# Optimization experiments

Measured on AMD Instinct MI355X. Metric: run time of the kernel, lower is better.

The kernel has to match this reference:

```python
import jax, jax.numpy as jnp
import numpy as np

C = 64          # num_channels
DEPTH = 9       # dilation_depth
REPEAT = 2      # dilation_repeat
K = 2           # kernel_size
DILATIONS = [2 ** j for _ in range(REPEAT) for j in range(DEPTH)]
L = len(DILATIONS)  # 18 gated layers


def causal_conv(x, w, b, dilation):
    # x: [B, Cin, T], w: [Cout, Cin, K] -> [B, Cout, T] with causal (left) padding
    pad = (w.shape[-1] - 1) * dilation
    y = jax.lax.conv_general_dilated(
        x, w, window_strides=(1,), padding=[(pad, 0)],
        rhs_dilation=(dilation,), dimension_numbers=("NCH", "OIH", "NCH"))
    return y + b[None, :, None]


def setup_inputs() -> dict:
    key = jax.random.key(0)
    ks = jax.random.split(key, 9)
    s = 0.1
    x = jax.random.normal(ks[0], (4, 1, 65536), dtype=jnp.float32)
    in_w = jax.random.normal(ks[1], (C, 1, 1), dtype=jnp.float32) * s
    in_b = jax.random.normal(ks[2], (C,), dtype=jnp.float32) * s
    hid_w = jax.random.normal(ks[3], (L, 2 * C, C, K), dtype=jnp.float32) * s
    hid_b = jax.random.normal(ks[4], (L, 2 * C), dtype=jnp.float32) * s
    res_w = jax.random.normal(ks[5], (L, C, C, 1), dtype=jnp.float32) * s
    res_b = jax.random.normal(ks[6], (L, C), dtype=jnp.float32) * s
    mix_w = jax.random.normal(ks[7], (1, C * L, 1), dtype=jnp.float32) * s
    mix_b = jax.random.normal(ks[8], (1,), dtype=jnp.float32) * s
    return {"x": x, "in_w": in_w, "in_b": in_b, "hid_w": hid_w, "hid_b": hid_b,
            "res_w": res_w, "res_b": res_b, "mix_w": mix_w, "mix_b": mix_b}


def reference(x, in_w, in_b, hid_w, hid_b, res_w, res_b, mix_w, mix_b):
    # Input 1x1 conv: [B,1,T] -> [B,C,T]
    out = causal_conv(x, in_w, in_b, 1)
    skips = []
    for i, d in enumerate(DILATIONS):
        xi = out
        h = causal_conv(xi, hid_w[i], hid_b[i], d)       # [B, 2C, T]
        gated = jnp.tanh(h[:, :C]) * jax.nn.sigmoid(h[:, C:])  # [B, C, T]
        skips.append(gated)
        out = causal_conv(gated, res_w[i], res_b[i], 1) + xi    # residual
    skip = jnp.concatenate(skips, axis=1)                # [B, C*L, T]
    return causal_conv(skip, mix_w, mix_b, 1)            # [B, 1, T]
```

## Files before the change

### kernel.cpp

```cpp
#include <hip/hip_runtime.h>
#include <hip/hip_bf16.h>
#include <math.h>

#define NCH 64
#define T_LEN 65536
#define NLAYER 18

typedef __attribute__((ext_vector_type(8))) short bf16x8;
typedef __attribute__((ext_vector_type(4))) short bf16x4;
typedef __attribute__((ext_vector_type(4))) float f32x4;

static __device__ __forceinline__ float bf2f(short s) {
    union { short u[2]; float f; } v;
    v.u[0] = 0; v.u[1] = s;
    return v.f;
}
static __device__ __forceinline__ short f2bf(float f) {
    __hip_bfloat16 h = __float2bfloat16(f);
    return *(short*)&h;
}

__global__ void convert_weights_kernel(const float* __restrict__ hid_w,
                                       const float* __restrict__ res_w,
                                       __hip_bfloat16* __restrict__ whid,
                                       __hip_bfloat16* __restrict__ wres) {
    int gid = blockIdx.x * 256 + threadIdx.x;
    if (gid < NLAYER * 128 * 128) {
        int l   = gid >> 14;
        int rem = gid & 16383;
        int o   = rem >> 7;
        int k   = rem & 127;
        float v = (k < 64)
            ? hid_w[((l * 128 + o) * 64 + k) * 2]
            : hid_w[((l * 128 + o) * 64 + (k - 64)) * 2 + 1];
        whid[gid] = __float2bfloat16(v);
    }
    if (gid < NLAYER * 64 * 64) {
        wres[gid] = __float2bfloat16(res_w[gid]);
    }
}

__global__ __launch_bounds__(256, 2) void fused6_kernel(
    const void* __restrict__ src,
    __hip_bfloat16* __restrict__ next,
    float* __restrict__ acc,
    const __hip_bfloat16* __restrict__ whid_all,
    const float* __restrict__ hb_all,
    const __hip_bfloat16* __restrict__ wres_all,
    const float* __restrict__ rb_all,
    const float* __restrict__ mix_w,
    const float* __restrict__ in_w,
    const float* __restrict__ in_b,
    int lbase, int is_first) {
    __shared__ __align__(16) __hip_bfloat16 A[192 * 72];
    __shared__ __align__(16) __hip_bfloat16 G[192 * 72];

    const int b    = blockIdx.x >> 9;
    const int widx = blockIdx.x & 511;
    const int t0   = widx << 7;
    const int tw   = t0 - 64;

    const int tid  = threadIdx.x;
    const int lane = tid & 63;
    const int w4   = tid >> 6;
    const int l15  = lane & 15;
    const int quad = lane >> 4;
    const int m0   = w4 * 16;
    const int rr   = tid >> 3;
    const int co   = (tid & 7) * 8;

    if (is_first) {
        const float* x = (const float*)src;
        float iw[8], ib[8];
#pragma unroll
        for (int j = 0; j < 8; ++j) { iw[j] = in_w[co + j]; ib[j] = in_b[co + j]; }
#pragma unroll
        for (int round = 0; round < 6; ++round) {
            int r  = round * 32 + rr;
            int gt = tw + r;
            bf16x8 v = {0, 0, 0, 0, 0, 0, 0, 0};
            if (gt >= 0) {
                float xv = x[(size_t)b * T_LEN + gt];
#pragma unroll
                for (int j = 0; j < 8; ++j) v[j] = f2bf(iw[j] * xv + ib[j]);
            }
            *(bf16x8*)(&A[r * 72 + co]) = v;
        }
    } else {
        const __hip_bfloat16* prev = (const __hip_bfloat16*)src;
#pragma unroll
        for (int round = 0; round < 6; ++round) {
            int r  = round * 32 + rr;
            int gt = tw + r;
            bf16x8 v = {0, 0, 0, 0, 0, 0, 0, 0};
            if (gt >= 0)
                v = *(const bf16x8*)(prev + ((size_t)b * T_LEN + gt) * NCH + co);
            *(bf16x8*)(&A[r * 72 + co]) = v;
        }
    }

    float skacc0 = 0.f, skacc1 = 0.f;

#pragma unroll 1
    for (int l = 0; l < 6; ++l) {
        const int d = 1 << l;
        const __hip_bfloat16* whid = whid_all + (size_t)(lbase + l) * 16384;
        const __hip_bfloat16* wres = wres_all + (size_t)(lbase + l) * 4096;
        const float* hb = hb_all + (lbase + l) * 128;
        const float* rb = rb_all + (lbase + l) * 64;
        const float* mw = mix_w + (lbase + l) * 64;

        bf16x8 aT[4], aS[4], aR[2];
        {
            const __hip_bfloat16* whT = whid + (size_t)(m0 + l15) * 128 + quad * 8;
            const __hip_bfloat16* whS = whT + 64 * 128;
#pragma unroll
            for (int k = 0; k < 4; ++k) {
                aT[k] = *(const bf16x8*)(whT + k * 32);
                aS[k] = *(const bf16x8*)(whS + k * 32);
            }
            const __hip_bfloat16* wrA = wres + (size_t)(m0 + l15) * 64 + quad * 8;
            aR[0] = *(const bf16x8*)(wrA);
            aR[1] = *(const bf16x8*)(wrA + 32);
        }
        f32x4 biasT, biasS, biasR;
#pragma unroll
        for (int r = 0; r < 4; ++r) {
            biasT[r] = hb[m0 + quad * 4 + r];
            biasS[r] = hb[64 + m0 + quad * 4 + r];
            biasR[r] = rb[m0 + quad * 4 + r];
        }
        float mwq[16];
#pragma unroll
        for (int k = 0; k < 4; ++k) {
            float4 m4 = *(const float4*)(mw + quad * 16 + k * 4);
            mwq[k * 4 + 0] = m4.x; mwq[k * 4 + 1] = m4.y;
            mwq[k * 4 + 2] = m4.z; mwq[k * 4 + 3] = m4.w;
        }

        __syncthreads();

#pragma unroll
        for (int ct = 0; ct < 3; ++ct) {
            f32x4 accT[4], accS[4];
#pragma unroll
            for (int nt = 0; nt < 4; ++nt) { accT[nt] = biasT; accS[nt] = biasS; }
#pragma unroll
            for (int ks = 0; ks < 4; ++ks) {
                const int koff = (ks & 1) * 32 + quad * 8;
#pragma unroll
                for (int nt = 0; nt < 4; ++nt) {
                    int trow = ct * 64 + nt * 16 + l15;
                    int prow = trow - d;  prow = prow < 0 ? 0 : prow;
                    int row  = (ks < 2) ? prow : trow;
                    bf16x8 bx = *(const bf16x8*)(&A[row * 72 + koff]);
                    accT[nt] = __builtin_amdgcn_mfma_f32_16x16x32_bf16(aT[ks], bx, accT[nt], 0, 0, 0);
                    accS[nt] = __builtin_amdgcn_mfma_f32_16x16x32_bf16(aS[ks], bx, accS[nt], 0, 0, 0);
                }
            }
#pragma unroll
            for (int nt = 0; nt < 4; ++nt) {
                int trow = ct * 64 + nt * 16 + l15;
                bf16x4 gv;
#pragma unroll
                for (int r = 0; r < 4; ++r) {
                    float e2 = __expf(2.f * accT[nt][r]);
                    float th = 1.f - 2.f * __builtin_amdgcn_rcpf(e2 + 1.f);
                    float sg = __builtin_amdgcn_rcpf(1.f + __expf(-accS[nt][r]));
                    gv[r] = f2bf(th * sg);
                }
                *(bf16x4*)(&G[trow * 72 + m0 + quad * 4]) = gv;
            }
        }
        __syncthreads();

#pragma unroll
        for (int ct = 0; ct < 3; ++ct) {
            f32x4 accR[4];
#pragma unroll
            for (int nt = 0; nt < 4; ++nt) accR[nt] = biasR;
#pragma unroll
            for (int ks = 0; ks < 2; ++ks) {
                const int koff = ks * 32 + quad * 8;
#pragma unroll
                for (int nt = 0; nt < 4; ++nt) {
                    int trow = ct * 64 + nt * 16 + l15;
                    bf16x8 bx = *(const bf16x8*)(&G[trow * 72 + koff]);
                    accR[nt] = __builtin_amdgcn_mfma_f32_16x16x32_bf16(aR[ks], bx, accR[nt], 0, 0, 0);
                }
            }
#pragma unroll
            for (int nt = 0; nt < 4; ++nt) {
                int trow = ct * 64 + nt * 16 + l15;
                bf16x4 old = *(const bf16x4*)(&A[trow * 72 + m0 + quad * 4]);
                bool ok = (tw + trow) >= 0;
                bf16x4 ov;
#pragma unroll
                for (int r = 0; r < 4; ++r) {
                    float v = accR[nt][r] + bf2f(old[r]);
                    ov[r] = f2bf(ok ? v : 0.f);
                }
                *(bf16x4*)(&A[trow * 72 + m0 + quad * 4]) = ov;
            }
        }

#pragma unroll
        for (int s = 0; s < 2; ++s) {
            int p = 64 + w4 * 32 + s * 16 + l15;
            bf16x8 g0 = *(const bf16x8*)(&G[p * 72 + quad * 16]);
            bf16x8 g1 = *(const bf16x8*)(&G[p * 72 + quad * 16 + 8]);
            float sv = 0.f;
#pragma unroll
            for (int j = 0; j < 8; ++j) {
                sv += mwq[j]     * bf2f(g0[j]);
                sv += mwq[8 + j] * bf2f(g1[j]);
            }
            if (s == 0) skacc0 += sv; else skacc1 += sv;
        }
    }
    __syncthreads();

#pragma unroll
    for (int round = 0; round < 4; ++round) {
        int pr = round * 32 + rr;
        *(bf16x8*)(next + ((size_t)b * T_LEN + t0 + pr) * NCH + co) =
            *(const bf16x8*)(&A[(pr + 64) * 72 + co]);
    }

    skacc0 += __shfl_xor(skacc0, 16, 64);
    skacc0 += __shfl_xor(skacc0, 32, 64);
    skacc1 += __shfl_xor(skacc1, 16, 64);
    skacc1 += __shfl_xor(skacc1, 32, 64);
    if (quad == 0) {
        acc[(size_t)b * T_LEN + t0 + w4 * 32 + l15]      += skacc0;
        acc[(size_t)b * T_LEN + t0 + w4 * 32 + 16 + l15] += skacc1;
    }
}

__global__ __launch_bounds__(256, 2) void layer_mfma_kernel(
    const __hip_bfloat16* __restrict__ prev,
    __hip_bfloat16* __restrict__ next,
    float* __restrict__ acc,
    const __hip_bfloat16* __restrict__ whid,
    const float* __restrict__ hb,
    const __hip_bfloat16* __restrict__ wres,
    const float* __restrict__ rb,
    const float* __restrict__ mw,
    int d) {
    __shared__ __align__(16) __hip_bfloat16 Xp[64 * 72];
    __shared__ __align__(16) __hip_bfloat16 Xc[64 * 72];
    __shared__ __align__(16) __hip_bfloat16 Gt[64 * 72];

    const int t0   = blockIdx.x << 6;
    const int tid  = threadIdx.x;
    const int lane = tid & 63;
    const int w4   = tid >> 6;
    const int l15  = lane & 15;
    const int quad = lane >> 4;
    const int m0   = w4 * 16;
    const int rr = tid >> 3;
    const int co = (tid & 7) * 8;

    bf16x8 aT[4], aS[4], aR[2];
    {
        const __hip_bfloat16* whT = whid + (size_t)(m0 + l15) * 128 + quad * 8;
        const __hip_bfloat16* whS = whT + 64 * 128;
#pragma unroll
        for (int k = 0; k < 4; ++k) {
            aT[k] = *(const bf16x8*)(whT + k * 32);
            aS[k] = *(const bf16x8*)(whS + k * 32);
        }
        const __hip_bfloat16* wrA = wres + (size_t)(m0 + l15) * 64 + quad * 8;
        aR[0] = *(const bf16x8*)(wrA);
        aR[1] = *(const bf16x8*)(wrA + 32);
    }
    f32x4 biasT, biasS, biasR;
#pragma unroll
    for (int r = 0; r < 4; ++r) {
        biasT[r] = hb[m0 + quad * 4 + r];
        biasS[r] = hb[64 + m0 + quad * 4 + r];
        biasR[r] = rb[m0 + quad * 4 + r];
    }
    float mwq[16];
#pragma unroll
    for (int j = 0; j < 16; ++j) mwq[j] = mw[quad * 16 + j];

    bf16x8 pc[2], pp[2];
#define LOAD_TILE(b)                                                          \
    do {                                                                      \
        const __hip_bfloat16* pb = prev + ((size_t)(b) * T_LEN + t0) * NCH;   \
        _Pragma("unroll")                                                     \
        for (int pass = 0; pass < 2; ++pass) {                                \
            int r = pass * 32 + rr;                                           \
            pc[pass] = *(const bf16x8*)(pb + r * NCH + co);                   \
            int tp = t0 + r - d;                                              \
            bf16x8 z = {0, 0, 0, 0, 0, 0, 0, 0};                              \
            pp[pass] = z;                                                     \
            if (tp >= 0)                                                      \
                pp[pass] = *(const bf16x8*)(prev +                            \
                    ((size_t)(b) * T_LEN + tp) * NCH + co);                   \
        }                                                                     \
    } while (0)

    LOAD_TILE(0);

#pragma unroll
    for (int b = 0; b < 4; ++b) {
#pragma unroll
        for (int pass = 0; pass < 2; ++pass) {
            int r = pass * 32 + rr;
            *(bf16x8*)(&Xc[r * 72 + co]) = pc[pass];
            *(bf16x8*)(&Xp[r * 72 + co]) = pp[pass];
        }
        __syncthreads();

        if (b < 3) LOAD_TILE(b + 1);

        f32x4 accT[4], accS[4];
#pragma unroll
        for (int nt = 0; nt < 4; ++nt) { accT[nt] = biasT; accS[nt] = biasS; }
#pragma unroll
        for (int ks = 0; ks < 4; ++ks) {
            const __hip_bfloat16* srcb = (ks < 2) ? Xp : Xc;
            const int kk = (ks & 1) * 32 + quad * 8;
#pragma unroll
            for (int nt = 0; nt < 4; ++nt) {
                bf16x8 bx = *(const bf16x8*)(&srcb[(nt * 16 + l15) * 72 + kk]);
                accT[nt] = __builtin_amdgcn_mfma_f32_16x16x32_bf16(aT[ks], bx, accT[nt], 0, 0, 0);
                accS[nt] = __builtin_amdgcn_mfma_f32_16x16x32_bf16(aS[ks], bx, accS[nt], 0, 0, 0);
            }
        }

#pragma unroll
        for (int nt = 0; nt < 4; ++nt) {
            int t = nt * 16 + l15;
#pragma unroll
            for (int r = 0; r < 4; ++r) {
                float e2 = __expf(2.f * accT[nt][r]);
                float th = 1.f - 2.f * __builtin_amdgcn_rcpf(e2 + 1.f);
                float sg = __builtin_amdgcn_rcpf(1.f + __expf(-accS[nt][r]));
                Gt[t * 72 + m0 + quad * 4 + r] = __float2bfloat16(th * sg);
            }
        }

        bf16x4 curres[4];
#pragma unroll
        for (int nt = 0; nt < 4; ++nt) {
            curres[nt] = *(const bf16x4*)(&Xc[(nt * 16 + l15) * 72 + m0 + quad * 4]);
        }
        __syncthreads();

        f32x4 accR[4];
#pragma unroll
        for (int nt = 0; nt < 4; ++nt) accR[nt] = biasR;
#pragma unroll
        for (int ks = 0; ks < 2; ++ks) {
            const int kk = ks * 32 + quad * 8;
#pragma unroll
            for (int nt = 0; nt < 4; ++nt) {
                bf16x8 bx = *(const bf16x8*)(&Gt[(nt * 16 + l15) * 72 + kk]);
                accR[nt] = __builtin_amdgcn_mfma_f32_16x16x32_bf16(aR[ks], bx, accR[nt], 0, 0, 0);
            }
        }

        __hip_bfloat16* nb = next + ((size_t)b * T_LEN + t0) * NCH;
#pragma unroll
        for (int nt = 0; nt < 4; ++nt) {
            int t = nt * 16 + l15;
            bf16x4 ov;
#pragma unroll
            for (int r = 0; r < 4; ++r) {
                ov[r] = f2bf(accR[nt][r] + bf2f(curres[nt][r]));
            }
            *(bf16x4*)(nb + t * NCH + m0 + quad * 4) = ov;
        }

        {
            int t = w4 * 16 + l15;
            bf16x8 g0 = *(const bf16x8*)(&Gt[t * 72 + quad * 16]);
            bf16x8 g1 = *(const bf16x8*)(&Gt[t * 72 + quad * 16 + 8]);
            float s = 0.f;
#pragma unroll
            for (int j = 0; j < 8; ++j) {
                s += mwq[j]     * bf2f(g0[j]);
                s += mwq[8 + j] * bf2f(g1[j]);
            }
            s += __shfl_xor(s, 16, 64);
            s += __shfl_xor(s, 32, 64);
            if (quad == 0)
                acc[(size_t)b * T_LEN + t0 + t] += s;
        }
    }
#undef LOAD_TILE
}

__global__ __launch_bounds__(256, 2) void last_layer_kernel(
    const __hip_bfloat16* __restrict__ prev,
    const float* __restrict__ acc,
    float* __restrict__ out,
    const __hip_bfloat16* __restrict__ whid,
    const float* __restrict__ hb,
    const float* __restrict__ mw,
    const float* __restrict__ mix_b,
    int d) {
    __shared__ __align__(16) __hip_bfloat16 Xp[64 * 72];
    __shared__ __align__(16) __hip_bfloat16 Xc[64 * 72];
    __shared__ float skb[4 * 64];

    const int t0   = blockIdx.x << 6;
    const int tid  = threadIdx.x;
    const int lane = tid & 63;
    const int w4   = tid >> 6;
    const int l15  = lane & 15;
    const int quad = lane >> 4;
    const int m0   = w4 * 16;
    const int rr = tid >> 3;
    const int co = (tid & 7) * 8;

    bf16x8 aT[4], aS[4];
    {
        const __hip_bfloat16* whT = whid + (size_t)(m0 + l15) * 128 + quad * 8;
        const __hip_bfloat16* whS = whT + 64 * 128;
#pragma unroll
        for (int k = 0; k < 4; ++k) {
            aT[k] = *(const bf16x8*)(whT + k * 32);
            aS[k] = *(const bf16x8*)(whS + k * 32);
        }
    }
    f32x4 biasT, biasS;
    float mwv[4];
#pragma unroll
    for (int r = 0; r < 4; ++r) {
        biasT[r] = hb[m0 + quad * 4 + r];
        biasS[r] = hb[64 + m0 + quad * 4 + r];
        mwv[r]   = mw[m0 + quad * 4 + r];
    }
    const float mb = mix_b[0];

    bf16x8 pc[2], pp[2];
#define LOAD_TILE(b)                                                          \
    do {                                                                      \
        const __hip_bfloat16* pb = prev + ((size_t)(b) * T_LEN + t0) * NCH;   \
        _Pragma("unroll")                                                     \
        for (int pass = 0; pass < 2; ++pass) {                                \
            int r = pass * 32 + rr;                                           \
            pc[pass] = *(const bf16x8*)(pb + r * NCH + co);                   \
            int tp = t0 + r - d;                                              \
            bf16x8 z = {0, 0, 0, 0, 0, 0, 0, 0};                              \
            pp[pass] = z;                                                     \
            if (tp >= 0)                                                      \
                pp[pass] = *(const bf16x8*)(prev +                            \
                    ((size_t)(b) * T_LEN + tp) * NCH + co);                   \
        }                                                                     \
    } while (0)

    LOAD_TILE(0);

#pragma unroll
    for (int b = 0; b < 4; ++b) {
#pragma unroll
        for (int pass = 0; pass < 2; ++pass) {
            int r = pass * 32 + rr;
            *(bf16x8*)(&Xc[r * 72 + co]) = pc[pass];
            *(bf16x8*)(&Xp[r * 72 + co]) = pp[pass];
        }
        __syncthreads();

        if (b < 3) LOAD_TILE(b + 1);

        f32x4 accT[4], accS[4];
#pragma unroll
        for (int nt = 0; nt < 4; ++nt) { accT[nt] = biasT; accS[nt] = biasS; }
#pragma unroll
        for (int ks = 0; ks < 4; ++ks) {
            const __hip_bfloat16* srcb = (ks < 2) ? Xp : Xc;
            const int kk = (ks & 1) * 32 + quad * 8;
#pragma unroll
            for (int nt = 0; nt < 4; ++nt) {
                bf16x8 bx = *(const bf16x8*)(&srcb[(nt * 16 + l15) * 72 + kk]);
                accT[nt] = __builtin_amdgcn_mfma_f32_16x16x32_bf16(aT[ks], bx, accT[nt], 0, 0, 0);
                accS[nt] = __builtin_amdgcn_mfma_f32_16x16x32_bf16(aS[ks], bx, accS[nt], 0, 0, 0);
            }
        }

#pragma unroll
        for (int nt = 0; nt < 4; ++nt) {
            float sv = 0.f;
#pragma unroll
            for (int r = 0; r < 4; ++r) {
                float e2 = __expf(2.f * accT[nt][r]);
                float th = 1.f - 2.f * __builtin_amdgcn_rcpf(e2 + 1.f);
                float sg = __builtin_amdgcn_rcpf(1.f + __expf(-accS[nt][r]));
                sv += mwv[r] * (th * sg);
            }
            sv += __shfl_xor(sv, 16, 64);
            sv += __shfl_xor(sv, 32, 64);
            if (quad == 0)
                skb[w4 * 64 + nt * 16 + l15] = sv;
        }
        __syncthreads();

        if (tid < 64) {
            float tot = skb[tid] + skb[64 + tid] + skb[128 + tid] + skb[192 + tid];
            out[(size_t)b * T_LEN + t0 + tid] =
                acc[(size_t)b * T_LEN + t0 + tid] + tot + mb;
        }
    }
#undef LOAD_TILE
}

extern "C" void kernel_launch(void* const* d_in, const int* in_sizes, int n_in,
                              void* d_out, int out_size, void* d_ws, size_t ws_size,
                              hipStream_t stream) {
    const float* x     = (const float*)d_in[0];
    const float* in_w  = (const float*)d_in[1];
    const float* in_b  = (const float*)d_in[2];
    const float* hid_w = (const float*)d_in[3];
    const float* hid_b = (const float*)d_in[4];
    const float* res_w = (const float*)d_in[5];
    const float* res_b = (const float*)d_in[6];
    const float* mix_w = (const float*)d_in[7];
    const float* mix_b = (const float*)d_in[8];
    float* out = (float*)d_out;

    const size_t act_elems = 4ull * T_LEN * NCH;
    __hip_bfloat16* actA = (__hip_bfloat16*)d_ws;
    __hip_bfloat16* actB = actA + act_elems;
    float* acc = (float*)(actB + act_elems);
    __hip_bfloat16* whid = (__hip_bfloat16*)(acc + 4ull * T_LEN);
    __hip_bfloat16* wres = whid + (size_t)NLAYER * 128 * 128;

    hipMemsetAsync(acc, 0, 4ull * T_LEN * sizeof(float), stream);

    convert_weights_kernel<<<1152, 256, 0, stream>>>(hid_w, res_w, whid, wres);

    fused6_kernel<<<2048, 256, 0, stream>>>(
        x, actA, acc, whid, hid_b, wres, res_b, mix_w, in_w, in_b, 0, 1);

    layer_mfma_kernel<<<1024, 256, 0, stream>>>(
        actA, actB, acc, whid + 6 * 16384, hid_b + 6 * 128,
        wres + 6 * 4096, res_b + 6 * 64, mix_w + 6 * 64, 64);
    layer_mfma_kernel<<<1024, 256, 0, stream>>>(
        actB, actA, acc, whid + 7 * 16384, hid_b + 7 * 128,
        wres + 7 * 4096, res_b + 7 * 64, mix_w + 7 * 64, 128);
    layer_mfma_kernel<<<1024, 256, 0, stream>>>(
        actA, actB, acc, whid + 8 * 16384, hid_b + 8 * 128,
        wres + 8 * 4096, res_b + 8 * 64, mix_w + 8 * 64, 256);

    fused6_kernel<<<2048, 256, 0, stream>>>(
        actB, actA, acc, whid, hid_b, wres, res_b, mix_w, in_w, in_b, 9, 0);

    layer_mfma_kernel<<<1024, 256, 0, stream>>>(
        actA, actB, acc, whid + 15 * 16384, hid_b + 15 * 128,
        wres + 15 * 4096, res_b + 15 * 64, mix_w + 15 * 64, 64);
    layer_mfma_kernel<<<1024, 256, 0, stream>>>(
        actB, actA, acc, whid + 16 * 16384, hid_b + 16 * 128,
        wres + 16 * 4096, res_b + 16 * 64, mix_w + 16 * 64, 128);

    last_layer_kernel<<<1024, 256, 0, stream>>>(
        actA, acc, out, whid + 17 * 16384, hid_b + 17 * 128,
        mix_w + 17 * 64, mix_b, 256);
}
```

Baseline: 556.0 us.

## Swizzle fused-kernel LDS tiles, merge gate reciprocals, raise occupancy bounds

Replaces the padded 72-element LDS row stride in the fused six-layer kernel with an unpadded 64-element layout using an XOR swizzle on 8-element chunks. This cuts LDS footprint and is meant to avoid bank conflicts. The tanh*sigmoid gate now uses a single reciprocal of a product, with clamping to avoid overflow. Launch bounds are raised to allow 3 or 4 blocks per CU, which may force register spilling.

```diff
diff --git a/kernel.cpp b/kernel.cpp
--- a/kernel.cpp
+++ b/kernel.cpp
@@ -18,6 +18,15 @@
 static __device__ __forceinline__ short f2bf(float f) {
     __hip_bfloat16 h = __float2bfloat16(f);
     return *(short*)&h;
+}
+static __device__ __forceinline__ float gate_fn(float x, float y) {
+    x = fminf(fmaxf(x, -15.f), 15.f);
+    float e2 = __expf(2.f * x);
+    float em = __expf(-y);
+    return (e2 - 1.f) * __builtin_amdgcn_rcpf((e2 + 1.f) * (1.f + em));
+}
+static __device__ __forceinline__ int sw(int row, int elem) {
+    return (row << 6) + ((((elem >> 3) ^ (row & 7)) << 3) | (elem & 7));
 }
 
 __global__ void convert_weights_kernel(const float* __restrict__ hid_w,
@@ -40,7 +49,7 @@
     }
 }
 
-__global__ __launch_bounds__(256, 2) void fused6_kernel(
+__global__ __launch_bounds__(256, 3) void fused6_kernel(
     const void* __restrict__ src,
     __hip_bfloat16* __restrict__ next,
     float* __restrict__ acc,
@@ -52,8 +61,8 @@
     const float* __restrict__ in_w,
     const float* __restrict__ in_b,
     int lbase, int is_first) {
-    __shared__ __align__(16) __hip_bfloat16 A[192 * 72];
-    __shared__ __align__(16) __hip_bfloat16 G[192 * 72];
+    __shared__ __align__(16) __hip_bfloat16 A[192 * 64];
+    __shared__ __align__(16) __hip_bfloat16 G[192 * 64];
 
     const int b    = blockIdx.x >> 9;
     const int widx = blockIdx.x & 511;
@@ -84,7 +93,7 @@
 #pragma unroll
                 for (int j = 0; j < 8; ++j) v[j] = f2bf(iw[j] * xv + ib[j]);
             }
-            *(bf16x8*)(&A[r * 72 + co]) = v;
+            *(bf16x8*)(&A[sw(r, co)]) = v;
         }
     } else {
         const __hip_bfloat16* prev = (const __hip_bfloat16*)src;
@@ -95,7 +104,7 @@
             bf16x8 v = {0, 0, 0, 0, 0, 0, 0, 0};
             if (gt >= 0)
                 v = *(const bf16x8*)(prev + ((size_t)b * T_LEN + gt) * NCH + co);
-            *(bf16x8*)(&A[r * 72 + co]) = v;
+            *(bf16x8*)(&A[sw(r, co)]) = v;
         }
     }
 
@@ -153,7 +162,7 @@
                     int trow = ct * 64 + nt * 16 + l15;
                     int prow = trow - d;  prow = prow < 0 ? 0 : prow;
                     int row  = (ks < 2) ? prow : trow;
-                    bf16x8 bx = *(const bf16x8*)(&A[row * 72 + koff]);
+                    bf16x8 bx = *(const bf16x8*)(&A[sw(row, koff)]);
                     accT[nt] = __builtin_amdgcn_mfma_f32_16x16x32_bf16(aT[ks], bx, accT[nt], 0, 0, 0);
                     accS[nt] = __builtin_amdgcn_mfma_f32_16x16x32_bf16(aS[ks], bx, accS[nt], 0, 0, 0);
                 }
@@ -164,12 +173,9 @@
                 bf16x4 gv;
 #pragma unroll
                 for (int r = 0; r < 4; ++r) {
-                    float e2 = __expf(2.f * accT[nt][r]);
-                    float th = 1.f - 2.f * __builtin_amdgcn_rcpf(e2 + 1.f);
-                    float sg = __builtin_amdgcn_rcpf(1.f + __expf(-accS[nt][r]));
-                    gv[r] = f2bf(th * sg);
+                    gv[r] = f2bf(gate_fn(accT[nt][r], accS[nt][r]));
                 }
-                *(bf16x4*)(&G[trow * 72 + m0 + quad * 4]) = gv;
+                *(bf16x4*)(&G[sw(trow, m0 + quad * 4)]) = gv;
             }
         }
         __syncthreads();
@@ -185,14 +191,15 @@
 #pragma unroll
                 for (int nt = 0; nt < 4; ++nt) {
                     int trow = ct * 64 + nt * 16 + l15;
-                    bf16x8 bx = *(const bf16x8*)(&G[trow * 72 + koff]);
+                    bf16x8 bx = *(const bf16x8*)(&G[sw(trow, koff)]);
                     accR[nt] = __builtin_amdgcn_mfma_f32_16x16x32_bf16(aR[ks], bx, accR[nt], 0, 0, 0);
                 }
             }
 #pragma unroll
             for (int nt = 0; nt < 4; ++nt) {
                 int trow = ct * 64 + nt * 16 + l15;
-                bf16x4 old = *(const bf16x4*)(&A[trow * 72 + m0 + quad * 4]);
+                int idx  = sw(trow, m0 + quad * 4);
+                bf16x4 old = *(const bf16x4*)(&A[idx]);
                 bool ok = (tw + trow) >= 0;
                 bf16x4 ov;
 #pragma unroll
@@ -200,15 +207,15 @@
                     float v = accR[nt][r] + bf2f(old[r]);
                     ov[r] = f2bf(ok ? v : 0.f);
                 }
-                *(bf16x4*)(&A[trow * 72 + m0 + quad * 4]) = ov;
+                *(bf16x4*)(&A[idx]) = ov;
             }
         }
 
 #pragma unroll
         for (int s = 0; s < 2; ++s) {
             int p = 64 + w4 * 32 + s * 16 + l15;
-            bf16x8 g0 = *(const bf16x8*)(&G[p * 72 + quad * 16]);
-            bf16x8 g1 = *(const bf16x8*)(&G[p * 72 + quad * 16 + 8]);
+            bf16x8 g0 = *(const bf16x8*)(&G[sw(p, quad * 16)]);
+            bf16x8 g1 = *(const bf16x8*)(&G[sw(p, quad * 16 + 8)]);
             float sv = 0.f;
 #pragma unroll
             for (int j = 0; j < 8; ++j) {
@@ -224,7 +231,7 @@
     for (int round = 0; round < 4; ++round) {
         int pr = round * 32 + rr;
         *(bf16x8*)(next + ((size_t)b * T_LEN + t0 + pr) * NCH + co) =
-            *(const bf16x8*)(&A[(pr + 64) * 72 + co]);
+            *(const bf16x8*)(&A[sw(pr + 64, co)]);
     }
 
     skacc0 += __shfl_xor(skacc0, 16, 64);
@@ -237,7 +244,7 @@
     }
 }
 
-__global__ __launch_bounds__(256, 2) void layer_mfma_kernel(
+__global__ __launch_bounds__(256, 4) void layer_mfma_kernel(
     const __hip_bfloat16* __restrict__ prev,
     __hip_bfloat16* __restrict__ next,
     float* __restrict__ acc,
@@ -336,10 +343,8 @@
             int t = nt * 16 + l15;
 #pragma unroll
             for (int r = 0; r < 4; ++r) {
-                float e2 = __expf(2.f * accT[nt][r]);
-                float th = 1.f - 2.f * __builtin_amdgcn_rcpf(e2 + 1.f);
-                float sg = __builtin_amdgcn_rcpf(1.f + __expf(-accS[nt][r]));
-                Gt[t * 72 + m0 + quad * 4 + r] = __float2bfloat16(th * sg);
+                Gt[t * 72 + m0 + quad * 4 + r] =
+                    __float2bfloat16(gate_fn(accT[nt][r], accS[nt][r]));
             }
         }
 
@@ -394,7 +399,7 @@
 #undef LOAD_TILE
 }
 
-__global__ __launch_bounds__(256, 2) void last_layer_kernel(
+__global__ __launch_bounds__(256, 4) void last_layer_kernel(
     const __hip_bfloat16* __restrict__ prev,
     const float* __restrict__ acc,
     float* __restrict__ out,
@@ -488,10 +493,7 @@
             float sv = 0.f;
 #pragma unroll
             for (int r = 0; r < 4; ++r) {
-                float e2 = __expf(2.f * accT[nt][r]);
-                float th = 1.f - 2.f * __builtin_amdgcn_rcpf(e2 + 1.f);
-                float sg = __builtin_amdgcn_rcpf(1.f + __expf(-accS[nt][r]));
-                sv += mwv[r] * (th * sg);
+                sv += mwv[r] * gate_fn(accT[nt][r], accS[nt][r]);
             }
             sv += __shfl_xor(sv, 16, 64);
             sv += __shfl_xor(sv, 32, 64);
```

New measurement: 666.7 us. +19.9%, slower.
